# Performance work log

Measured on AMD Instinct MI355X. Metric: run time of the kernel, lower is better.

Reference implementation:

```python
import jax, jax.numpy as jnp
import numpy as np


def setup_inputs() -> dict:
    key = jax.random.key(0)
    x = jax.random.normal(key, (4, 4, 32, 256, 256), dtype=jnp.float32)
    return {"x": x}


def reference(x):
    # NonMaximaSuppression3d with kernel_size=(3,3,3) fast path:
    # a voxel survives iff it is strictly greater than all 26 neighbors;
    # border voxels (no full neighborhood) are always suppressed.
    B, CH, D, H, W = x.shape
    ct = x[..., 1:-1, 1:-1, 1:-1]  # interior centers [B,CH,D-2,H-2,W-2]
    mask_inner = jnp.ones(ct.shape, dtype=bool)
    for dz in range(3):
        for dy in range(3):
            for dx in range(3):
                if (dz, dy, dx) == (1, 1, 1):
                    continue
                neigh = x[..., dz:D - 2 + dz, dy:H - 2 + dy, dx:W - 2 + dx]
                mask_inner = mask_inner & (ct > neigh)
    mask = jnp.zeros(x.shape, dtype=bool).at[..., 1:-1, 1:-1, 1:-1].set(mask_inner)
    return x * mask.astype(x.dtype)
```

## Files before the change

### kernel.cpp

```cpp
#include <hip/hip_runtime.h>


constexpr int W  = 256;
constexpr int H  = 256;
constexpr int D  = 32;
constexpr int SH = W;
constexpr int SD = W * H;
constexpr int HC = 16;
constexpr int HCHUNKS = H / HC;
constexpr int BC = 16;

__global__ __launch_bounds__(256) void nms3d_kernel(const float* __restrict__ x,
                                                    float* __restrict__ out) {
    const int wid  = (blockIdx.x << 2) | (threadIdx.x >> 6);
    const int lane = threadIdx.x & 63;
    const int hc   = wid & (HCHUNKS - 1);
    const int d    = (wid >> 4) & (D - 1);
    const int bc   = wid >> 9;
    const int col  = bc * (D * SD) + d * SD + (lane << 2);
    const int h0   = hc * HC;

    const float4 zero = make_float4(0.f, 0.f, 0.f, 0.f);

    if (d == 0 || d == D - 1) {
        #pragma unroll
        for (int h = 0; h < HC; ++h)
            *(float4*)(out + col + (h0 + h) * SH) = zero;
        return;
    }

    const int h_begin = (h0 == 0) ? 1 : h0;
    const int h_end   = (h0 + HC == H) ? (H - 2) : (h0 + HC - 1);
    if (h0 == 0)      *(float4*)(out + col) = zero;
    if (h0 + HC == H) *(float4*)(out + col + (H - 1) * SH) = zero;

    float4 v[3][3];
    float  lm[3][3], rp[3][3];

    #pragma unroll
    for (int s = 0; s < 2; ++s) {
        const int h = h_begin - 1 + s;
        #pragma unroll
        for (int dz = 0; dz < 3; ++dz) {
            float4 t = *(const float4*)(x + col + (dz - 1) * SD + h * SH);
            v[dz][s]  = t;
            lm[dz][s] = __shfl_up(t.w, 1);
            rp[dz][s] = __shfl_down(t.x, 1);
        }
    }

    for (int h = h_begin; h <= h_end; ++h) {
        #pragma unroll
        for (int dz = 0; dz < 3; ++dz) {
            float4 t = *(const float4*)(x + col + (dz - 1) * SD + (h + 1) * SH);
            v[dz][2]  = t;
            lm[dz][2] = __shfl_up(t.w, 1);
            rp[dz][2] = __shfl_down(t.x, 1);
        }

        const float4 c = v[1][1];
        float n0 = -INFINITY, n1 = -INFINITY, n2 = -INFINITY, n3 = -INFINITY;

        #pragma unroll
        for (int dz = 0; dz < 3; ++dz) {
            #pragma unroll
            for (int s = 0; s < 3; ++s) {
                const float4 r = v[dz][s];
                const float  l = lm[dz][s];
                const float  q = rp[dz][s];
                if (dz == 1 && s == 1) {
                    n0 = fmaxf(n0, fmaxf(l,   r.y));
                    n1 = fmaxf(n1, fmaxf(r.x, r.z));
                    n2 = fmaxf(n2, fmaxf(r.y, r.w));
                    n3 = fmaxf(n3, fmaxf(r.z, q));
                } else {
                    n0 = fmaxf(n0, fmaxf(fmaxf(l,   r.x), r.y));
                    n1 = fmaxf(n1, fmaxf(fmaxf(r.x, r.y), r.z));
                    n2 = fmaxf(n2, fmaxf(fmaxf(r.y, r.z), r.w));
                    n3 = fmaxf(n3, fmaxf(fmaxf(r.z, r.w), q));
                }
            }
        }

        float4 o;
        o.x = (lane > 0  && c.x > n0) ? c.x : 0.f;
        o.y = (c.y > n1) ? c.y : 0.f;
        o.z = (c.z > n2) ? c.z : 0.f;
        o.w = (lane < 63 && c.w > n3) ? c.w : 0.f;
        *(float4*)(out + col + h * SH) = o;

        #pragma unroll
        for (int dz = 0; dz < 3; ++dz) {
            v[dz][0]  = v[dz][1];  v[dz][1]  = v[dz][2];
            lm[dz][0] = lm[dz][1]; lm[dz][1] = lm[dz][2];
            rp[dz][0] = rp[dz][1]; rp[dz][1] = rp[dz][2];
        }
    }
}

extern "C" void kernel_launch(void* const* d_in, const int* in_sizes, int n_in,
                              void* d_out, int out_size, void* d_ws, size_t ws_size,
                              hipStream_t stream) {
    const float* x = (const float*)d_in[0];
    float* out = (float*)d_out;
    const int grid = (BC * D * HCHUNKS) / 4;
    nms3d_kernel<<<grid, 256, 0, stream>>>(x, out);
}
```

Measured before the change: 242.4 us.

## Prefetch next row, use nontemporal stores, and halve H chunk size

Each row's three depth slices are now loaded one iteration ahead into a prefetch register set, so global load latency overlaps the current row's max computation. Output stores switch to nontemporal stores to avoid polluting cache with write-only data. The H chunk shrinks from 16 to 8 rows, doubling the wave count for more parallelism at the cost of more redundant halo row loads. The launch grid is derived from HCHUNKS and so adjusts automatically.

```diff
diff --git a/kernel.cpp b/kernel.cpp
--- a/kernel.cpp
+++ b/kernel.cpp
@@ -1,12 +1,14 @@
 #include <hip/hip_runtime.h>
 
+
+typedef float v4f __attribute__((ext_vector_type(4)));
 
 constexpr int W  = 256;
 constexpr int H  = 256;
 constexpr int D  = 32;
 constexpr int SH = W;
 constexpr int SD = W * H;
-constexpr int HC = 16;
+constexpr int HC = 8;
 constexpr int HCHUNKS = H / HC;
 constexpr int BC = 16;
 
@@ -15,85 +17,98 @@
     const int wid  = (blockIdx.x << 2) | (threadIdx.x >> 6);
     const int lane = threadIdx.x & 63;
     const int hc   = wid & (HCHUNKS - 1);
-    const int d    = (wid >> 4) & (D - 1);
-    const int bc   = wid >> 9;
+    const int d    = (wid >> 5) & (D - 1);
+    const int bc   = wid >> 10;
     const int col  = bc * (D * SD) + d * SD + (lane << 2);
     const int h0   = hc * HC;
 
-    const float4 zero = make_float4(0.f, 0.f, 0.f, 0.f);
+    const v4f zero = (v4f){0.f, 0.f, 0.f, 0.f};
 
     if (d == 0 || d == D - 1) {
         #pragma unroll
         for (int h = 0; h < HC; ++h)
-            *(float4*)(out + col + (h0 + h) * SH) = zero;
+            __builtin_nontemporal_store(zero, (v4f*)(out + col + (h0 + h) * SH));
         return;
     }
 
     const int h_begin = (h0 == 0) ? 1 : h0;
     const int h_end   = (h0 + HC == H) ? (H - 2) : (h0 + HC - 1);
-    if (h0 == 0)      *(float4*)(out + col) = zero;
-    if (h0 + HC == H) *(float4*)(out + col + (H - 1) * SH) = zero;
+    if (h0 == 0)      __builtin_nontemporal_store(zero, (v4f*)(out + col));
+    if (h0 + HC == H) __builtin_nontemporal_store(zero, (v4f*)(out + col + (H - 1) * SH));
 
-    float4 v[3][3];
-    float  lm[3][3], rp[3][3];
+    v4f s0[3], s1[3], pf[3];
+    float lm0[3], rp0[3], lm1[3], rp1[3];
 
     #pragma unroll
-    for (int s = 0; s < 2; ++s) {
-        const int h = h_begin - 1 + s;
-        #pragma unroll
-        for (int dz = 0; dz < 3; ++dz) {
-            float4 t = *(const float4*)(x + col + (dz - 1) * SD + h * SH);
-            v[dz][s]  = t;
-            lm[dz][s] = __shfl_up(t.w, 1);
-            rp[dz][s] = __shfl_down(t.x, 1);
-        }
+    for (int dz = 0; dz < 3; ++dz) {
+        const float* base = x + col + (dz - 1) * SD;
+        v4f a = *(const v4f*)(base + (h_begin - 1) * SH);
+        v4f b = *(const v4f*)(base + h_begin * SH);
+        pf[dz] = *(const v4f*)(base + (h_begin + 1) * SH);
+        s0[dz] = a; lm0[dz] = __shfl_up(a.w, 1); rp0[dz] = __shfl_down(a.x, 1);
+        s1[dz] = b; lm1[dz] = __shfl_up(b.w, 1); rp1[dz] = __shfl_down(b.x, 1);
     }
 
     for (int h = h_begin; h <= h_end; ++h) {
+        v4f s2[3]; float lm2[3], rp2[3];
         #pragma unroll
         for (int dz = 0; dz < 3; ++dz) {
-            float4 t = *(const float4*)(x + col + (dz - 1) * SD + (h + 1) * SH);
-            v[dz][2]  = t;
-            lm[dz][2] = __shfl_up(t.w, 1);
-            rp[dz][2] = __shfl_down(t.x, 1);
+            v4f t = pf[dz];
+            s2[dz] = t;
+            lm2[dz] = __shfl_up(t.w, 1);
+            rp2[dz] = __shfl_down(t.x, 1);
         }
 
-        const float4 c = v[1][1];
+        int hp = h + 2; if (hp > H - 1) hp = H - 1;
+        #pragma unroll
+        for (int dz = 0; dz < 3; ++dz)
+            pf[dz] = *(const v4f*)(x + col + (dz - 1) * SD + hp * SH);
+
+        const v4f c = s1[1];
         float n0 = -INFINITY, n1 = -INFINITY, n2 = -INFINITY, n3 = -INFINITY;
 
         #pragma unroll
         for (int dz = 0; dz < 3; ++dz) {
-            #pragma unroll
-            for (int s = 0; s < 3; ++s) {
-                const float4 r = v[dz][s];
-                const float  l = lm[dz][s];
-                const float  q = rp[dz][s];
-                if (dz == 1 && s == 1) {
-                    n0 = fmaxf(n0, fmaxf(l,   r.y));
-                    n1 = fmaxf(n1, fmaxf(r.x, r.z));
-                    n2 = fmaxf(n2, fmaxf(r.y, r.w));
-                    n3 = fmaxf(n3, fmaxf(r.z, q));
-                } else {
-                    n0 = fmaxf(n0, fmaxf(fmaxf(l,   r.x), r.y));
-                    n1 = fmaxf(n1, fmaxf(fmaxf(r.x, r.y), r.z));
-                    n2 = fmaxf(n2, fmaxf(fmaxf(r.y, r.z), r.w));
-                    n3 = fmaxf(n3, fmaxf(fmaxf(r.z, r.w), q));
-                }
+            {
+                const v4f r = s0[dz]; const float l = lm0[dz], q = rp0[dz];
+                n0 = fmaxf(n0, fmaxf(fmaxf(l, r.x), r.y));
+                n1 = fmaxf(n1, fmaxf(fmaxf(r.x, r.y), r.z));
+                n2 = fmaxf(n2, fmaxf(fmaxf(r.y, r.z), r.w));
+                n3 = fmaxf(n3, fmaxf(fmaxf(r.z, r.w), q));
+            }
+            if (dz == 1) {
+                const v4f r = s1[1]; const float l = lm1[1], q = rp1[1];
+                n0 = fmaxf(n0, fmaxf(l, r.y));
+                n1 = fmaxf(n1, fmaxf(r.x, r.z));
+                n2 = fmaxf(n2, fmaxf(r.y, r.w));
+                n3 = fmaxf(n3, fmaxf(r.z, q));
+            } else {
+                const v4f r = s1[dz]; const float l = lm1[dz], q = rp1[dz];
+                n0 = fmaxf(n0, fmaxf(fmaxf(l, r.x), r.y));
+                n1 = fmaxf(n1, fmaxf(fmaxf(r.x, r.y), r.z));
+                n2 = fmaxf(n2, fmaxf(fmaxf(r.y, r.z), r.w));
+                n3 = fmaxf(n3, fmaxf(fmaxf(r.z, r.w), q));
+            }
+            {
+                const v4f r = s2[dz]; const float l = lm2[dz], q = rp2[dz];
+                n0 = fmaxf(n0, fmaxf(fmaxf(l, r.x), r.y));
+                n1 = fmaxf(n1, fmaxf(fmaxf(r.x, r.y), r.z));
+                n2 = fmaxf(n2, fmaxf(fmaxf(r.y, r.z), r.w));
+                n3 = fmaxf(n3, fmaxf(fmaxf(r.z, r.w), q));
             }
         }
 
-        float4 o;
+        v4f o;
         o.x = (lane > 0  && c.x > n0) ? c.x : 0.f;
         o.y = (c.y > n1) ? c.y : 0.f;
         o.z = (c.z > n2) ? c.z : 0.f;
         o.w = (lane < 63 && c.w > n3) ? c.w : 0.f;
-        *(float4*)(out + col + h * SH) = o;
+        __builtin_nontemporal_store(o, (v4f*)(out + col + h * SH));
 
         #pragma unroll
         for (int dz = 0; dz < 3; ++dz) {
-            v[dz][0]  = v[dz][1];  v[dz][1]  = v[dz][2];
-            lm[dz][0] = lm[dz][1]; lm[dz][1] = lm[dz][2];
-            rp[dz][0] = rp[dz][1]; rp[dz][1] = rp[dz][2];
+            s0[dz] = s1[dz]; lm0[dz] = lm1[dz]; rp0[dz] = rp1[dz];
+            s1[dz] = s2[dz]; lm1[dz] = lm2[dz]; rp1[dz] = rp2[dz];
         }
     }
 }
```

Result: faster. 235.0 us (-3.1%).
